# Kernel optimization log

Hardware: AMD Instinct MI355X
Metric: run time of the kernel (lower is better)

The kernel has to match this reference:

```python
import jax, jax.numpy as jnp
import numpy as np

B, L, DIM, NH = 2, 2048, 1024, 16
HD = DIM // NH

def setup_inputs() -> dict:
    key = jax.random.key(0)
    ks = jax.random.split(key, 7)
    s = 1.0 / np.sqrt(DIM)
    x = jax.random.normal(ks[0], (B, L, DIM), dtype=jnp.float32)
    pos_bias = jax.random.normal(ks[1], (B, NH, L, L), dtype=jnp.float32)
    mask = jax.random.randint(ks[2], (B, L), 0, 2, dtype=jnp.int32)
    wq = jax.random.normal(ks[3], (DIM, DIM), dtype=jnp.float32) * s
    wk = jax.random.normal(ks[4], (DIM, DIM), dtype=jnp.float32) * s
    wv = jax.random.normal(ks[5], (DIM, DIM), dtype=jnp.float32) * s
    wo = jax.random.normal(ks[6], (DIM, DIM), dtype=jnp.float32) * s
    return {"x": x, "pos_bias": pos_bias, "mask": mask, "wq": wq, "wk": wk, "wv": wv, "wo": wo}

def reference(x, pos_bias, mask, wq, wk, wv, wo):
    b, l, _ = x.shape
    # projections (bias-free linears); reshape to [B, L, n, c]
    q = (x @ wq).reshape(b, l, NH, HD)
    k = (x @ wk).reshape(b, l, NH, HD)
    v = (x @ wv).reshape(b, l, NH, HD)
    # additive bias: pos_bias, with masked positions set to dtype min (T5: no 1/sqrt(d) scaling)
    neg = jnp.finfo(x.dtype).min
    attn_bias = jnp.where(mask[:, None, None, :] == 0, neg, pos_bias)
    scores = jnp.einsum('binc,bjnc->bnij', q, k) + attn_bias  # [B, n, L, L]
    attn = jax.nn.softmax(scores, axis=-1)
    out = jnp.einsum('bnij,bjnc->binc', attn, v).reshape(b, l, DIM)
    return out @ wo
```

## Files before the change

kernel.cpp:

```cpp
#include <hip/hip_runtime.h>
#include <cmath>

typedef _Float16 half8 __attribute__((ext_vector_type(8)));
typedef _Float16 half4 __attribute__((ext_vector_type(4)));
typedef float f32x4 __attribute__((ext_vector_type(4)));

#define NEGBIG (-3.4028235e38f)

__global__ void cast4_kernel(const float* __restrict__ in, _Float16* __restrict__ out, int n) {
    int i = (blockIdx.x * 256 + threadIdx.x) * 4;
    if (i < n) {
        float4 v = *(const float4*)&in[i];
        half4 o = { (_Float16)v.x, (_Float16)v.y, (_Float16)v.z, (_Float16)v.w };
        *(half4*)&out[i] = o;
    }
}

__global__ void transpose_cast_kernel(const float* __restrict__ W, _Float16* __restrict__ Wt) {
    __shared__ float tile[32][33];
    int bx = blockIdx.x * 32;
    int by = blockIdx.y * 32;
    int tx = threadIdx.x & 31, ty = threadIdx.x >> 5;
    #pragma unroll
    for (int r = 0; r < 32; r += 8)
        tile[ty + r][tx] = W[(size_t)(bx + ty + r) * 1024 + by + tx];
    __syncthreads();
    #pragma unroll
    for (int r = 0; r < 32; r += 8)
        Wt[(size_t)(by + ty + r) * 1024 + bx + tx] = (_Float16)tile[tx][ty + r];
}

__global__ __launch_bounds__(256)
void gemm_qkv_kernel(const _Float16* __restrict__ X,
                     const _Float16* __restrict__ WqT, const _Float16* __restrict__ WkT,
                     const _Float16* __restrict__ WvT,
                     _Float16* __restrict__ Qh, _Float16* __restrict__ Kh, _Float16* __restrict__ VTh)
{
    const int z = blockIdx.z;
    const _Float16* __restrict__ Bt = (z == 0) ? WqT : (z == 1) ? WkT : WvT;
    _Float16* __restrict__ out      = (z == 0) ? Qh  : (z == 1) ? Kh  : VTh;

    __shared__ _Float16 Asb[128][40];
    __shared__ _Float16 Bsb[128][40];

    const int tid = threadIdx.x;
    const int bm = blockIdx.x * 128;
    const int bn = blockIdx.y * 128;
    const int wave = tid >> 6, lane = tid & 63;
    const int wm = (wave >> 1) * 64, wn = (wave & 1) * 64;
    const int quad = lane >> 4, l16 = lane & 15;

    f32x4 acc[4][4] = {};

    for (int k0 = 0; k0 < 1024; k0 += 32) {
        #pragma unroll
        for (int c = 0; c < 2; ++c) {
            int chunk = tid + c * 256;
            int row = chunk >> 2;
            int kc  = (chunk & 3) * 8;
            *(half8*)&Asb[row][kc] = *(const half8*)&X [(size_t)(bm + row) * 1024 + k0 + kc];
            *(half8*)&Bsb[row][kc] = *(const half8*)&Bt[(size_t)(bn + row) * 1024 + k0 + kc];
        }
        __syncthreads();
        half8 af[4], bf[4];
        #pragma unroll
        for (int mt = 0; mt < 4; ++mt) af[mt] = *(const half8*)&Asb[wm + mt*16 + l16][quad * 8];
        #pragma unroll
        for (int nt = 0; nt < 4; ++nt) bf[nt] = *(const half8*)&Bsb[wn + nt*16 + l16][quad * 8];
        #pragma unroll
        for (int mt = 0; mt < 4; ++mt)
            #pragma unroll
            for (int nt = 0; nt < 4; ++nt)
                acc[mt][nt] = __builtin_amdgcn_mfma_f32_16x16x32_f16(af[mt], bf[nt], acc[mt][nt], 0, 0, 0);
        __syncthreads();
    }

    #pragma unroll
    for (int mt = 0; mt < 4; ++mt) {
        #pragma unroll
        for (int nt = 0; nt < 4; ++nt) {
            #pragma unroll
            for (int r = 0; r < 4; ++r) {
                int m = bm + wm + mt * 16 + quad * 4 + r;
                int n = bn + wn + nt * 16 + l16;
                _Float16 hv = (_Float16)acc[mt][nt][r];
                int bb = m >> 11, ll = m & 2047, hh = n >> 6, dd = n & 63;
                if (z < 2)
                    out[(((size_t)(bb * 16 + hh)) * 2048 + ll) * 64 + dd] = hv;
                else
                    out[(((size_t)(bb * 16 + hh)) * 64 + dd) * 2048 + ll] = hv;
            }
        }
    }
}

__device__ __forceinline__ float rowmax16(float v) {
    #pragma unroll
    for (int off = 1; off < 16; off <<= 1) v = fmaxf(v, __shfl_xor(v, off));
    return v;
}
__device__ __forceinline__ float rowsum16(float v) {
    #pragma unroll
    for (int off = 1; off < 16; off <<= 1) v += __shfl_xor(v, off);
    return v;
}

__global__ __launch_bounds__(256)
void flash_attn_kernel(const _Float16* __restrict__ Qh, const _Float16* __restrict__ Kh,
                       const _Float16* __restrict__ VTh, const float* __restrict__ bias,
                       const int* __restrict__ mask, _Float16* __restrict__ AO)
{
    const int qt = blockIdx.x, h = blockIdx.y, b = blockIdx.z;
    const int tid = threadIdx.x, wave = tid >> 6, lane = tid & 63;
    const int quad = lane >> 4, l16 = lane & 15;

    __shared__ _Float16 Kt[64][72];
    __shared__ _Float16 Vt[64][72];
    __shared__ _Float16 Pw[4][16][72];

    const size_t head = (size_t)(b * 16 + h) * 2048 * 64;
    const int i_base = qt * 64 + wave * 16;
    const int ig0 = i_base + quad * 4;

    half8 qf0 = *(const half8*)&Qh[head + (size_t)(i_base + l16) * 64 + quad * 8];
    half8 qf1 = *(const half8*)&Qh[head + (size_t)(i_base + l16) * 64 + 32 + quad * 8];

    float m_r[4] = { -INFINITY, -INFINITY, -INFINITY, -INFINITY };
    float l_r[4] = {};
    f32x4 o[4] = {};

    for (int j0 = 0; j0 < 2048; j0 += 64) {
        #pragma unroll
        for (int c = 0; c < 2; ++c) {
            int chunk = tid + c * 256;
            int row = chunk >> 3;
            int dc  = (chunk & 7) * 8;
            *(half8*)&Kt[row][dc] = *(const half8*)&Kh [head + (size_t)(j0 + row) * 64 + dc];
            *(half8*)&Vt[row][dc] = *(const half8*)&VTh[head + (size_t)row * 2048 + j0 + dc];
        }
        __syncthreads();

        float sreg[4][4];
        #pragma unroll
        for (int jt = 0; jt < 4; ++jt) {
            half8 kf0 = *(const half8*)&Kt[jt * 16 + l16][quad * 8];
            half8 kf1 = *(const half8*)&Kt[jt * 16 + l16][32 + quad * 8];
            f32x4 s = {};
            s = __builtin_amdgcn_mfma_f32_16x16x32_f16(qf0, kf0, s, 0, 0, 0);
            s = __builtin_amdgcn_mfma_f32_16x16x32_f16(qf1, kf1, s, 0, 0, 0);
            int jg = j0 + jt * 16 + l16;
            int mv = mask[b * 2048 + jg];
            const float* bp = bias + ((size_t)((b * 16 + h) * 2048 + ig0)) * 2048 + jg;
            #pragma unroll
            for (int r = 0; r < 4; ++r) {
                float bv = bp[(size_t)r * 2048];
                sreg[jt][r] = s[r] + (mv ? bv : NEGBIG);
            }
        }

        float alpha[4];
        #pragma unroll
        for (int r = 0; r < 4; ++r) {
            float mx = fmaxf(fmaxf(sreg[0][r], sreg[1][r]), fmaxf(sreg[2][r], sreg[3][r]));
            mx = rowmax16(mx);
            float mnew = fmaxf(m_r[r], mx);
            alpha[r] = __expf(m_r[r] - mnew);
            m_r[r] = mnew;
            float ps = 0.f;
            #pragma unroll
            for (int jt = 0; jt < 4; ++jt) {
                float p = __expf(sreg[jt][r] - mnew);
                Pw[wave][quad * 4 + r][jt * 16 + l16] = (_Float16)p;
                ps += p;
            }
            ps = rowsum16(ps);
            l_r[r] = l_r[r] * alpha[r] + ps;
        }
        #pragma unroll
        for (int nt = 0; nt < 4; ++nt)
            #pragma unroll
            for (int r = 0; r < 4; ++r)
                o[nt][r] *= alpha[r];

        half8 pf0 = *(const half8*)&Pw[wave][l16][quad * 8];
        half8 pf1 = *(const half8*)&Pw[wave][l16][32 + quad * 8];
        #pragma unroll
        for (int nt = 0; nt < 4; ++nt) {
            half8 vf0 = *(const half8*)&Vt[nt * 16 + l16][quad * 8];
            half8 vf1 = *(const half8*)&Vt[nt * 16 + l16][32 + quad * 8];
            o[nt] = __builtin_amdgcn_mfma_f32_16x16x32_f16(pf0, vf0, o[nt], 0, 0, 0);
            o[nt] = __builtin_amdgcn_mfma_f32_16x16x32_f16(pf1, vf1, o[nt], 0, 0, 0);
        }
        __syncthreads();
    }

    #pragma unroll
    for (int nt = 0; nt < 4; ++nt) {
        #pragma unroll
        for (int r = 0; r < 4; ++r) {
            float val = o[nt][r] / l_r[r];
            AO[(size_t)(b * 2048 + i_base + quad * 4 + r) * 1024 + h * 64 + nt * 16 + l16] = (_Float16)val;
        }
    }
}

__global__ __launch_bounds__(256)
void gemm_out_kernel(const _Float16* __restrict__ A, const _Float16* __restrict__ Bt,
                     float* __restrict__ C)
{
    __shared__ _Float16 Asb[128][40];
    __shared__ _Float16 Bsb[128][40];

    const int tid = threadIdx.x;
    const int bm = blockIdx.x * 128;
    const int bn = blockIdx.y * 128;
    const int wave = tid >> 6, lane = tid & 63;
    const int wm = (wave >> 1) * 64, wn = (wave & 1) * 64;
    const int quad = lane >> 4, l16 = lane & 15;

    f32x4 acc[4][4] = {};

    for (int k0 = 0; k0 < 1024; k0 += 32) {
        #pragma unroll
        for (int c = 0; c < 2; ++c) {
            int chunk = tid + c * 256;
            int row = chunk >> 2;
            int kc  = (chunk & 3) * 8;
            *(half8*)&Asb[row][kc] = *(const half8*)&A [(size_t)(bm + row) * 1024 + k0 + kc];
            *(half8*)&Bsb[row][kc] = *(const half8*)&Bt[(size_t)(bn + row) * 1024 + k0 + kc];
        }
        __syncthreads();
        half8 af[4], bf[4];
        #pragma unroll
        for (int mt = 0; mt < 4; ++mt) af[mt] = *(const half8*)&Asb[wm + mt*16 + l16][quad * 8];
        #pragma unroll
        for (int nt = 0; nt < 4; ++nt) bf[nt] = *(const half8*)&Bsb[wn + nt*16 + l16][quad * 8];
        #pragma unroll
        for (int mt = 0; mt < 4; ++mt)
            #pragma unroll
            for (int nt = 0; nt < 4; ++nt)
                acc[mt][nt] = __builtin_amdgcn_mfma_f32_16x16x32_f16(af[mt], bf[nt], acc[mt][nt], 0, 0, 0);
        __syncthreads();
    }

    #pragma unroll
    for (int mt = 0; mt < 4; ++mt)
        #pragma unroll
        for (int nt = 0; nt < 4; ++nt)
            #pragma unroll
            for (int r = 0; r < 4; ++r) {
                int m = bm + wm + mt * 16 + quad * 4 + r;
                int n = bn + wn + nt * 16 + l16;
                C[(size_t)m * 1024 + n] = acc[mt][nt][r];
            }
}

extern "C" void kernel_launch(void* const* d_in, const int* in_sizes, int n_in,
                              void* d_out, int out_size, void* d_ws, size_t ws_size,
                              hipStream_t stream)
{
    const float* x    = (const float*)d_in[0];
    const float* bias = (const float*)d_in[1];
    const int*   mask = (const int*)d_in[2];
    const float* wq   = (const float*)d_in[3];
    const float* wk   = (const float*)d_in[4];
    const float* wv   = (const float*)d_in[5];
    const float* wo   = (const float*)d_in[6];
    float* out = (float*)d_out;

    char* ws = (char*)d_ws;
    const size_t MB = 1024 * 1024;
    _Float16* x_h = (_Float16*)(ws + 0);
    _Float16* AO  = x_h;
    _Float16* wqT = (_Float16*)(ws + 8 * MB);
    _Float16* wkT = (_Float16*)(ws + 10 * MB);
    _Float16* wvT = (_Float16*)(ws + 12 * MB);
    _Float16* woT = (_Float16*)(ws + 14 * MB);
    _Float16* Qh  = (_Float16*)(ws + 16 * MB);
    _Float16* Kh  = (_Float16*)(ws + 24 * MB);
    _Float16* VTh = (_Float16*)(ws + 32 * MB);

    cast4_kernel<<<4096, 256, 0, stream>>>(x, x_h, 4096 * 1024);
    dim3 tg(32, 32);
    transpose_cast_kernel<<<tg, 256, 0, stream>>>(wq, wqT);
    transpose_cast_kernel<<<tg, 256, 0, stream>>>(wk, wkT);
    transpose_cast_kernel<<<tg, 256, 0, stream>>>(wv, wvT);
    transpose_cast_kernel<<<tg, 256, 0, stream>>>(wo, woT);

    gemm_qkv_kernel<<<dim3(32, 8, 3), 256, 0, stream>>>(x_h, wqT, wkT, wvT, Qh, Kh, VTh);
    flash_attn_kernel<<<dim3(32, 16, 2), 256, 0, stream>>>(Qh, Kh, VTh, bias, mask, AO);
    gemm_out_kernel<<<dim3(32, 8), 256, 0, stream>>>(AO, woT, out);
}
```

Baseline: 838.3 us.

## Prefetch K/V/bias tiles into registers and stage masked bias in shared memory

The flash attention loop now issues the global loads for the next K, V, bias and mask tile into registers right after the barrier, so they overlap with the current tile's compute. Bias is loaded as coalesced float4 rows and the mask is applied once while writing to a shared-memory buffer, replacing scattered per-lane strided bias reads. MFMA sections are wrapped in s_setprio to favour matrix issue. The QKV projection GEMM for V swaps its MFMA operands so its transposed stores are contiguous along the sequence dimension. These changes raise register and LDS usage, which may reduce occupancy.

```diff
diff --git a/kernel.cpp b/kernel.cpp
--- a/kernel.cpp
+++ b/kernel.cpp
@@ -67,28 +67,50 @@
         for (int mt = 0; mt < 4; ++mt) af[mt] = *(const half8*)&Asb[wm + mt*16 + l16][quad * 8];
         #pragma unroll
         for (int nt = 0; nt < 4; ++nt) bf[nt] = *(const half8*)&Bsb[wn + nt*16 + l16][quad * 8];
-        #pragma unroll
-        for (int mt = 0; mt < 4; ++mt)
-            #pragma unroll
-            for (int nt = 0; nt < 4; ++nt)
-                acc[mt][nt] = __builtin_amdgcn_mfma_f32_16x16x32_f16(af[mt], bf[nt], acc[mt][nt], 0, 0, 0);
-        __syncthreads();
-    }
-
-    #pragma unroll
-    for (int mt = 0; mt < 4; ++mt) {
-        #pragma unroll
-        for (int nt = 0; nt < 4; ++nt) {
-            #pragma unroll
-            for (int r = 0; r < 4; ++r) {
-                int m = bm + wm + mt * 16 + quad * 4 + r;
-                int n = bn + wn + nt * 16 + l16;
-                _Float16 hv = (_Float16)acc[mt][nt][r];
-                int bb = m >> 11, ll = m & 2047, hh = n >> 6, dd = n & 63;
-                if (z < 2)
+        if (z == 2) {
+            #pragma unroll
+            for (int mt = 0; mt < 4; ++mt)
+                #pragma unroll
+                for (int nt = 0; nt < 4; ++nt)
+                    acc[mt][nt] = __builtin_amdgcn_mfma_f32_16x16x32_f16(bf[nt], af[mt], acc[mt][nt], 0, 0, 0);
+        } else {
+            #pragma unroll
+            for (int mt = 0; mt < 4; ++mt)
+                #pragma unroll
+                for (int nt = 0; nt < 4; ++nt)
+                    acc[mt][nt] = __builtin_amdgcn_mfma_f32_16x16x32_f16(af[mt], bf[nt], acc[mt][nt], 0, 0, 0);
+        }
+        __syncthreads();
+    }
+
+    if (z < 2) {
+        #pragma unroll
+        for (int mt = 0; mt < 4; ++mt) {
+            #pragma unroll
+            for (int nt = 0; nt < 4; ++nt) {
+                #pragma unroll
+                for (int r = 0; r < 4; ++r) {
+                    int m = bm + wm + mt * 16 + quad * 4 + r;
+                    int n = bn + wn + nt * 16 + l16;
+                    _Float16 hv = (_Float16)acc[mt][nt][r];
+                    int bb = m >> 11, ll = m & 2047, hh = n >> 6, dd = n & 63;
                     out[(((size_t)(bb * 16 + hh)) * 2048 + ll) * 64 + dd] = hv;
-                else
+                }
+            }
+        }
+    } else {
+        #pragma unroll
+        for (int mt = 0; mt < 4; ++mt) {
+            #pragma unroll
+            for (int nt = 0; nt < 4; ++nt) {
+                #pragma unroll
+                for (int r = 0; r < 4; ++r) {
+                    int n = bn + wn + nt * 16 + quad * 4 + r;
+                    int m = bm + wm + mt * 16 + l16;
+                    _Float16 hv = (_Float16)acc[mt][nt][r];
+                    int bb = m >> 11, ll = m & 2047, hh = n >> 6, dd = n & 63;
                     out[(((size_t)(bb * 16 + hh)) * 64 + dd) * 2048 + ll] = hv;
+                }
             }
         }
     }
@@ -116,11 +138,13 @@
 
     __shared__ _Float16 Kt[64][72];
     __shared__ _Float16 Vt[64][72];
+    __shared__ float    Bs[64][68];
     __shared__ _Float16 Pw[4][16][72];
 
     const size_t head = (size_t)(b * 16 + h) * 2048 * 64;
     const int i_base = qt * 64 + wave * 16;
-    const int ig0 = i_base + quad * 4;
+    const float* __restrict__ bias_base = bias + ((size_t)((b * 16 + h) * 2048 + qt * 64)) * 2048;
+    const int* __restrict__ mask_base = mask + b * 2048;
 
     half8 qf0 = *(const half8*)&Qh[head + (size_t)(i_base + l16) * 64 + quad * 8];
     half8 qf1 = *(const half8*)&Qh[head + (size_t)(i_base + l16) * 64 + 32 + quad * 8];
@@ -129,33 +153,63 @@
     float l_r[4] = {};
     f32x4 o[4] = {};
 
+    const int kv_row = tid >> 3;
+    const int kv_dc  = (tid & 7) * 8;
+    const int b_row0 = tid >> 4;
+    const int b_col  = (tid & 15) * 4;
+
+    half8 kreg[2], vreg[2];
+    f32x4 breg[4];
+    int4  mreg;
+
+    auto prefetch = [&](int j0) {
+        #pragma unroll
+        for (int c = 0; c < 2; ++c) {
+            int row = kv_row + c * 32;
+            kreg[c] = *(const half8*)&Kh [head + (size_t)(j0 + row) * 64 + kv_dc];
+            vreg[c] = *(const half8*)&VTh[head + (size_t)row * 2048 + j0 + kv_dc];
+        }
+        mreg = *(const int4*)&mask_base[j0 + b_col];
+        #pragma unroll
+        for (int c = 0; c < 4; ++c)
+            breg[c] = *(const f32x4*)&bias_base[(size_t)(b_row0 + c * 16) * 2048 + j0 + b_col];
+    };
+
+    prefetch(0);
+
     for (int j0 = 0; j0 < 2048; j0 += 64) {
         #pragma unroll
         for (int c = 0; c < 2; ++c) {
-            int chunk = tid + c * 256;
-            int row = chunk >> 3;
-            int dc  = (chunk & 7) * 8;
-            *(half8*)&Kt[row][dc] = *(const half8*)&Kh [head + (size_t)(j0 + row) * 64 + dc];
-            *(half8*)&Vt[row][dc] = *(const half8*)&VTh[head + (size_t)row * 2048 + j0 + dc];
-        }
-        __syncthreads();
-
+            int row = kv_row + c * 32;
+            *(half8*)&Kt[row][kv_dc] = kreg[c];
+            *(half8*)&Vt[row][kv_dc] = vreg[c];
+        }
+        #pragma unroll
+        for (int c = 0; c < 4; ++c) {
+            float* dst = &Bs[b_row0 + c * 16][b_col];
+            dst[0] = mreg.x ? breg[c][0] : NEGBIG;
+            dst[1] = mreg.y ? breg[c][1] : NEGBIG;
+            dst[2] = mreg.z ? breg[c][2] : NEGBIG;
+            dst[3] = mreg.w ? breg[c][3] : NEGBIG;
+        }
+        __syncthreads();
+
+        if (j0 + 64 < 2048) prefetch(j0 + 64);
+
+        const int iw = wave * 16 + quad * 4;
         float sreg[4][4];
         #pragma unroll
         for (int jt = 0; jt < 4; ++jt) {
             half8 kf0 = *(const half8*)&Kt[jt * 16 + l16][quad * 8];
             half8 kf1 = *(const half8*)&Kt[jt * 16 + l16][32 + quad * 8];
             f32x4 s = {};
+            __builtin_amdgcn_s_setprio(1);
             s = __builtin_amdgcn_mfma_f32_16x16x32_f16(qf0, kf0, s, 0, 0, 0);
             s = __builtin_amdgcn_mfma_f32_16x16x32_f16(qf1, kf1, s, 0, 0, 0);
-            int jg = j0 + jt * 16 + l16;
-            int mv = mask[b * 2048 + jg];
-            const float* bp = bias + ((size_t)((b * 16 + h) * 2048 + ig0)) * 2048 + jg;
-            #pragma unroll
-            for (int r = 0; r < 4; ++r) {
-                float bv = bp[(size_t)r * 2048];
-                sreg[jt][r] = s[r] + (mv ? bv : NEGBIG);
-            }
+            __builtin_amdgcn_s_setprio(0);
+            #pragma unroll
+            for (int r = 0; r < 4; ++r)
+                sreg[jt][r] = s[r] + Bs[iw + r][jt * 16 + l16];
         }
 
         float alpha[4];
@@ -188,8 +242,10 @@
         for (int nt = 0; nt < 4; ++nt) {
             half8 vf0 = *(const half8*)&Vt[nt * 16 + l16][quad * 8];
             half8 vf1 = *(const half8*)&Vt[nt * 16 + l16][32 + quad * 8];
+            __builtin_amdgcn_s_setprio(1);
             o[nt] = __builtin_amdgcn_mfma_f32_16x16x32_f16(pf0, vf0, o[nt], 0, 0, 0);
             o[nt] = __builtin_amdgcn_mfma_f32_16x16x32_f16(pf1, vf1, o[nt], 0, 0, 0);
+            __builtin_amdgcn_s_setprio(0);
         }
         __syncthreads();
     }
```

After: 846.4 us. About the same (+1.0%).
